# Optimization experiments

Measured on AMD Instinct MI355X. Metric: run time of the kernel, lower is better.

The kernel has to match this reference:

```python
import jax, jax.numpy as jnp
import numpy as np

NUM_HEADS = 4


def setup_inputs() -> dict:
    key = jax.random.key(0)
    ks = jax.random.split(key, 4)
    B, C, H, W = 8, 128, 128, 128
    x = jax.random.normal(ks[0], (B, C, H, W), dtype=jnp.float32)
    w_qkv = jax.random.normal(ks[1], (3 * C, C), dtype=jnp.float32) * 0.05
    w_proj = jax.random.normal(ks[2], (C, C), dtype=jnp.float32) * 0.05
    w_dw = jax.random.normal(ks[3], (C, 1, 3, 3), dtype=jnp.float32) * 0.1
    gamma = jnp.asarray(0.1, dtype=jnp.float32)
    return {"x": x, "w_qkv": w_qkv, "w_proj": w_proj, "w_dw": w_dw, "gamma": gamma}


def reference(x, w_qkv, w_proj, w_dw, gamma):
    B, C, H, W = x.shape
    h = NUM_HEADS
    d = C // h
    scale = d ** (-0.5)

    # 1x1 conv qkv: [B,3C,H,W]
    qkv = jnp.einsum('oc,bchw->bohw', w_qkv, x)
    # split and reshape to [B,h,H,W,d]; channel index = head*d + dim
    def to_heads(t):
        return t.reshape(B, h, d, H, W).transpose(0, 1, 3, 4, 2)
    q = to_heads(qkv[:, :C])
    k = to_heads(qkv[:, C:2 * C])
    v = to_heads(qkv[:, 2 * C:])

    # H-axis attention: attend along W within each row i
    attn_h = jnp.einsum('bhijd,bhizd->bhijz', q * scale, k)  # [B,h,H,W,W]
    idx_w = jnp.arange(W, dtype=jnp.float32)
    decay_w = jnp.exp(-gamma * jnp.abs(idx_w[:, None] - idx_w[None, :]))  # [W,W]
    attn_h = jax.nn.softmax(attn_h, axis=-1) * decay_w
    out_h = jnp.einsum('bhijz,bhizd->bhijd', attn_h, v)  # [B,h,H,W,d]

    # W-axis attention: attend along H within each column
    qw = q.transpose(0, 1, 3, 2, 4)  # [B,h,W,H,d]
    kw = k.transpose(0, 1, 3, 2, 4)
    vw = v.transpose(0, 1, 3, 2, 4)
    attn_w = jnp.einsum('bhwjd,bhwzd->bhwjz', qw * scale, kw)  # [B,h,W,H,H]
    idx_h = jnp.arange(H, dtype=jnp.float32)
    decay_h = jnp.exp(-gamma * jnp.abs(idx_h[:, None] - idx_h[None, :]))  # [H,H]
    attn_w = jax.nn.softmax(attn_w, axis=-1) * decay_h
    out_w = jnp.einsum('bhwjz,bhwzd->bhwjd', attn_w, vw).transpose(0, 1, 3, 2, 4)

    out = out_h + out_w  # [B,h,H,W,d]
    # back to [B,C,H,W], channel = head*d + dim
    out = out.transpose(0, 1, 4, 2, 3).reshape(B, C, H, W)

    # LePE: depthwise 3x3 conv (replaces out, matching original code)
    out = jax.lax.conv_general_dilated(
        out, w_dw, window_strides=(1, 1), padding='SAME',
        feature_group_count=C,
        dimension_numbers=('NCHW', 'OIHW', 'NCHW'))

    # 1x1 proj
    out = jnp.einsum('oc,bchw->bohw', w_proj, out)
    return out
```

## Files before the change

kernel.cpp:

```cpp
#include <hip/hip_runtime.h>

typedef unsigned short u16;
typedef unsigned int   u32;
typedef short bf16x8 __attribute__((ext_vector_type(8)));
typedef float f32x4  __attribute__((ext_vector_type(4)));
typedef float f32x2  __attribute__((ext_vector_type(2)));

#define B_   8
#define C_   128
#define H_   128
#define W_   128
#define NH   4
#define D_   32
#define HW_  16384
#define SCALE 0.17677669529663687f
#define SCL2E 0.2550437602866803f

__device__ __forceinline__ float bf2f_u(u16 u) { union { u32 i; float f; } x; x.i = ((u32)u) << 16; return x.f; }
__device__ __forceinline__ float bflo(u32 u)   { union { u32 i; float f; } x; x.i = u << 16; return x.f; }
__device__ __forceinline__ float bfhi(u32 u)   { union { u32 i; float f; } x; x.i = u & 0xffff0000u; return x.f; }
__device__ __forceinline__ u16   f2bf(float f) {
  union { float f; u32 i; } x; x.f = f;
  u32 i = x.i;
  return (u16)((i + 0x7fffu + ((i >> 16) & 1u)) >> 16);
}
__device__ __forceinline__ u32 pk2(float a, float b) {
  return (u32)f2bf(a) | ((u32)f2bf(b) << 16);
}
__device__ __forceinline__ u32 cvtpk(float a, float b) {
  u32 r;
  asm("v_cvt_pk_bf16_f32 %0, %1, %2" : "=v"(r) : "v"(a), "v"(b));
  return r;
}
__device__ __forceinline__ bf16x8 ld_frag_g(const u16* p) {
  union { uint4 u; bf16x8 f; } c; c.u = *(const uint4*)p; return c.f;
}

__global__ __launch_bounds__(256) void k_wcvt2(const float* __restrict__ wq,
                                               const float* __restrict__ wp,
                                               u16* __restrict__ dq,
                                               u16* __restrict__ dp) {
  int i = blockIdx.x * 256 + threadIdx.x;
  const float* src; u16* dst; int j;
  if (i < 12288) { src = wq; dst = dq; j = i; }
  else           { src = wp; dst = dp; j = i - 12288; }
  float4 v = ((const float4*)src)[j];
  uint2 st; st.x = pk2(v.x, v.y); st.y = pk2(v.z, v.w);
  *(uint2*)(dst + (size_t)j * 4) = st;
}

__global__ __launch_bounds__(256) void k_qkv(const float* __restrict__ x,
                                             const u16* __restrict__ wqb,
                                             u16* __restrict__ qkvb) {
  __shared__ u32 tile[8704];
  const int tid = threadIdx.x, w = tid >> 6, lane = tid & 63;
  const int c16 = lane & 15, rg = lane >> 4;
  const int b = blockIdx.z;
  const int P0 = blockIdx.x * 128;
  const float* sb = x + (size_t)b * C_ * HW_ + P0;

  #pragma unroll
  for (int ci = 0; ci < 4; ++ci) {
    int cp = 16 * w + 4 * ci + rg;
    #pragma unroll
    for (int ph = 0; ph < 2; ++ph) {
      int p = 4 * c16 + 64 * ph;
      const float* r0 = sb + (size_t)(2 * cp) * HW_ + p;
      float4 a  = *(const float4*)r0;
      float4 bb = *(const float4*)(r0 + HW_);
      tile[(p + 0) * 65 + cp] = pk2(a.x, bb.x);
      tile[(p + 1) * 65 + cp] = pk2(a.y, bb.y);
      tile[(p + 2) * 65 + cp] = pk2(a.z, bb.z);
      tile[(p + 3) * 65 + cp] = pk2(a.w, bb.w);
    }
  }
  __syncthreads();

  const int pw = w * 32;
  bf16x8 bfr[2][4];
  #pragma unroll
  for (int nt = 0; nt < 2; ++nt)
    #pragma unroll
    for (int kk = 0; kk < 4; ++kk) {
      int p = pw + nt * 16 + c16;
      int cp0 = kk * 16 + rg * 4;
      union { u32 d[4]; bf16x8 f; } u;
      u.d[0] = tile[p * 65 + cp0];
      u.d[1] = tile[p * 65 + cp0 + 1];
      u.d[2] = tile[p * 65 + cp0 + 2];
      u.d[3] = tile[p * 65 + cp0 + 3];
      bfr[nt][kk] = u.f;
    }
  __syncthreads();

  u32* eb = tile + w * 544;

  const int p0 = P0 + pw;
  const f32x4 zero = {0.f, 0.f, 0.f, 0.f};
  #pragma unroll 1
  for (int pass = 0; pass < 3; ++pass) {
    {
      const u16* wsrc = wqb + (size_t)pass * 16384;
      #pragma unroll
      for (int j = 0; j < 8; ++j) {
        int idx = tid + 256 * j;
        uint4 v = *(const uint4*)(wsrc + idx * 8);
        *(uint4*)(tile + (idx >> 4) * 68 + (idx & 15) * 4) = v;
      }
    }
    __syncthreads();

    f32x4 acc[8][2];
    #pragma unroll
    for (int mt = 0; mt < 8; ++mt) { acc[mt][0] = zero; acc[mt][1] = zero; }

    #pragma unroll
    for (int kk = 0; kk < 4; ++kk) {
      #pragma unroll
      for (int mt = 0; mt < 8; ++mt) {
        union { uint4 u; bf16x8 f; } afu;
        afu.u = *(const uint4*)(tile + (mt * 16 + c16) * 68 + kk * 16 + rg * 4);
        acc[mt][0] = __builtin_amdgcn_mfma_f32_16x16x32_bf16(afu.f, bfr[0][kk], acc[mt][0], 0, 0, 0);
        acc[mt][1] = __builtin_amdgcn_mfma_f32_16x16x32_bf16(afu.f, bfr[1][kk], acc[mt][1], 0, 0, 0);
      }
    }
    __syncthreads();

    u16* ob = qkvb + (size_t)pass * ((size_t)B_ * NH * HW_ * D_);
    #pragma unroll
    for (int h = 0; h < 4; ++h) {
      #pragma unroll
      for (int m2 = 0; m2 < 2; ++m2) {
        #pragma unroll
        for (int nt = 0; nt < 2; ++nt) {
          f32x4 oa = acc[2 * h + m2][nt];
          int pixl = nt * 16 + c16;
          int dp = m2 * 8 + rg * 2;
          eb[pixl * 17 + dp]     = cvtpk(oa[0], oa[1]);
          eb[pixl * 17 + dp + 1] = cvtpk(oa[2], oa[3]);
        }
      }
      #pragma unroll
      for (int s = 0; s < 2; ++s) {
        int pixl = s * 16 + (lane >> 2);
        const u32* src = eb + pixl * 17 + (lane & 3) * 4;
        uint4 v; v.x = src[0]; v.y = src[1]; v.z = src[2]; v.w = src[3];
        *(uint4*)(ob + ((size_t)(b * NH + h) * HW_ + p0 + pixl) * 32 + (lane & 3) * 8) = v;
      }
    }
    __syncthreads();
  }
}

__global__ __launch_bounds__(256) void k_proj(const u16* __restrict__ cv,
                                              const u16* __restrict__ wpb,
                                              float* __restrict__ out) {
  __shared__ u32 tile[8704];
  const int tid = threadIdx.x, w = tid >> 6, lane = tid & 63;
  const int c16 = lane & 15, rg = lane >> 4;
  const int b = blockIdx.z;
  const int P0 = blockIdx.x * 128;
  const u16* sb = cv + (size_t)b * C_ * HW_ + P0;

  #pragma unroll
  for (int ci = 0; ci < 4; ++ci) {
    int cp = 16 * w + 4 * ci + rg;
    #pragma unroll
    for (int ph = 0; ph < 2; ++ph) {
      int p = 4 * c16 + 64 * ph;
      const u16* r0 = sb + (size_t)(2 * cp) * HW_ + p;
      uint2 a  = *(const uint2*)r0;
      uint2 bb = *(const uint2*)(r0 + HW_);
      tile[(p + 0) * 65 + cp] = (a.x & 0xffffu) | (bb.x << 16);
      tile[(p + 1) * 65 + cp] = (a.x >> 16)     | (bb.x & 0xffff0000u);
      tile[(p + 2) * 65 + cp] = (a.y & 0xffffu) | (bb.y << 16);
      tile[(p + 3) * 65 + cp] = (a.y >> 16)     | (bb.y & 0xffff0000u);
    }
  }
  __syncthreads();

  const int pw = w * 32;
  bf16x8 bfr[2][4];
  #pragma unroll
  for (int nt = 0; nt < 2; ++nt)
    #pragma unroll
    for (int kk = 0; kk < 4; ++kk) {
      int p = pw + nt * 16 + c16;
      int cp0 = kk * 16 + rg * 4;
      union { u32 d[4]; bf16x8 f; } u;
      u.d[0] = tile[p * 65 + cp0];
      u.d[1] = tile[p * 65 + cp0 + 1];
      u.d[2] = tile[p * 65 + cp0 + 2];
      u.d[3] = tile[p * 65 + cp0 + 3];
      bfr[nt][kk] = u.f;
    }
  __syncthreads();

  u32* eb = tile + w * 544;

  #pragma unroll
  for (int j = 0; j < 8; ++j) {
    int idx = tid + 256 * j;
    uint4 v = *(const uint4*)(wpb + idx * 8);
    *(uint4*)(tile + (idx >> 4) * 68 + (idx & 15) * 4) = v;
  }
  __syncthreads();

  const int p0 = P0 + pw;
  const f32x4 zero = {0.f, 0.f, 0.f, 0.f};
  f32x4 acc[8][2];
  #pragma unroll
  for (int mt = 0; mt < 8; ++mt) { acc[mt][0] = zero; acc[mt][1] = zero; }

  #pragma unroll
  for (int kk = 0; kk < 4; ++kk) {
    #pragma unroll
    for (int mt = 0; mt < 8; ++mt) {
      union { uint4 u; bf16x8 f; } afu;
      afu.u = *(const uint4*)(tile + (mt * 16 + c16) * 68 + kk * 16 + rg * 4);
      acc[mt][0] = __builtin_amdgcn_mfma_f32_16x16x32_bf16(afu.f, bfr[0][kk], acc[mt][0], 0, 0, 0);
      acc[mt][1] = __builtin_amdgcn_mfma_f32_16x16x32_bf16(afu.f, bfr[1][kk], acc[mt][1], 0, 0, 0);
    }
  }
  __syncthreads();

  float* ob = out + (size_t)b * C_ * HW_;
  #pragma unroll
  for (int mt = 0; mt < 8; ++mt) {
    #pragma unroll
    for (int nt = 0; nt < 2; ++nt) {
      f32x4 oa = acc[mt][nt];
      int pixl = nt * 16 + c16;
      #pragma unroll
      for (int r = 0; r < 4; ++r) {
        union { float f; u32 u; } cu; cu.f = oa[r];
        eb[(rg * 4 + r) * 33 + pixl] = cu.u;
      }
    }
    #pragma unroll
    for (int s = 0; s < 2; ++s) {
      int ol = s * 8 + (lane >> 3);
      int px = (lane & 7) * 4;
      const u32* src = eb + ol * 33 + px;
      uint4 v; v.x = src[0]; v.y = src[1]; v.z = src[2]; v.w = src[3];
      *(uint4*)(ob + (size_t)(mt * 16 + ol) * HW_ + p0 + px) = v;
    }
  }
}

__global__ __launch_bounds__(256) void k_attn_mfma(const u16* __restrict__ qb,
                                                   const u16* __restrict__ kb,
                                                   const u16* __restrict__ vb,
                                                   const float* __restrict__ gp,
                                                   u16* __restrict__ houtb,
                                                   u16* __restrict__ woutb) {
  __shared__ u32 lds[4][16 * 68 + 32 * 18];
  const int tid  = threadIdx.x;
  const int w    = tid >> 6;
  const int lane = tid & 63;
  const int head = blockIdx.y & 3;
  const int axis = blockIdx.y >> 2;
  const int b    = blockIdx.z;
  const int line = blockIdx.x * 4 + w;
  u32* vt = &lds[w][0];
  u32* pt = &lds[w][0];
  u32* ot = &lds[w][16 * 68];
  const size_t base = (size_t)(b * NH + head) * HW_ * D_;
  const float g = gp[0];
  const int c16 = lane & 15, rg = lane >> 4;
  const size_t pstride = axis ? (size_t)128 * D_ : (size_t)D_;
  const size_t lbase   = base + (size_t)line * (axis ? D_ : 128 * D_);

  u32 v0r[16], v1r[16];
  {
    const u16* v0p = vb + lbase + (size_t)(2 * lane) * pstride;
    const u16* v1p = v0p + pstride;
    #pragma unroll
    for (int t = 0; t < 4; ++t) {
      *(uint4*)&v0r[4 * t] = *(const uint4*)(v0p + 8 * t);
      *(uint4*)&v1r[4 * t] = *(const uint4*)(v1p + 8 * t);
    }
  }

  bf16x8 kf[8];
  #pragma unroll
  for (int nt = 0; nt < 8; ++nt)
    kf[nt] = ld_frag_g(kb + lbase + (size_t)(nt * 16 + c16) * pstride + rg * 8);

  bf16x8 vf[2][4];
  #pragma unroll
  for (int ph = 0; ph < 2; ++ph) {
    #pragma unroll
    for (int dw = 0; dw < 8; ++dw) {
      u32 a = v0r[ph * 8 + dw], bq = v1r[ph * 8 + dw];
      u32 lo = (a & 0xffffu) | (bq << 16);
      u32 hi = (a >> 16) | (bq & 0xffff0000u);
      vt[(2 * dw) * 68 + lane]     = lo;
      vt[(2 * dw + 1) * 68 + lane] = hi;
    }
    #pragma unroll
    for (int t = 0; t < 4; ++t) {
      union { uint4 u; bf16x8 f; } c;
      c.u = *(const uint4*)(vt + c16 * 68 + t * 16 + rg * 4);
      vf[ph][t] = c.f;
    }
  }

  const float R1v  = __expf(-g),        Ri1v  = __expf(g);
  const float R12v = __expf(-12.f * g), Ri12v = __expf(12.f * g);
  const float R16v = __expf(-16.f * g), Ri16v = __expf(16.f * g);
  const f32x2 R1p   = {R1v,  Ri1v};
  const f32x2 R12p  = {R12v, Ri12v};
  const f32x2 R16ip = {Ri16v, R16v};
  float t0 = (float)(rg * 4 - c16);
  f32x2 F2 = {__expf(-g * t0), __expf(g * t0)};

  u16* ob = axis ? woutb : houtb;
  const f32x4 zero = {0.f, 0.f, 0.f, 0.f};

  bf16x8 qf = ld_frag_g(qb + lbase + (size_t)c16 * pstride + rg * 8);

  #pragma unroll 1
  for (int mt = 0; mt < 8; ++mt) {
    int mtn = mt < 7 ? mt + 1 : 7;
    bf16x8 qf_n = ld_frag_g(qb + lbase + (size_t)(mtn * 16 + c16) * pstride + rg * 8);

    f32x4 sa[8];
    __builtin_amdgcn_s_setprio(1);
    #pragma unroll
    for (int nt = 0; nt < 8; ++nt)
      sa[nt] = __builtin_amdgcn_mfma_f32_16x16x32_bf16(kf[nt], qf, zero, 0, 0, 0);
    __builtin_amdgcn_s_setprio(0);

    f32x2 l2 = {0.f, 0.f};
    #pragma unroll
    for (int nt = 0; nt < 8; ++nt) {
      f32x4 s4 = sa[nt] * SCL2E;
      float e0 = __builtin_amdgcn_exp2f(s4[0]);
      float e1 = __builtin_amdgcn_exp2f(s4[1]);
      float e2 = __builtin_amdgcn_exp2f(s4[2]);
      float e3 = __builtin_amdgcn_exp2f(s4[3]);
      sa[nt][0] = e0; sa[nt][1] = e1; sa[nt][2] = e2; sa[nt][3] = e3;
      l2 += (f32x2){e0, e1};
      l2 += (f32x2){e2, e3};
    }
    float l = l2[0] + l2[1];
    l += __shfl_xor(l, 16);
    l += __shfl_xor(l, 32);
    float linv = __builtin_amdgcn_rcpf(l);

    f32x2 ffi = F2 * linv;
    #pragma unroll
    for (int nt = 0; nt < 8; ++nt) {
      float d0 = fminf(ffi[0], ffi[1]); ffi *= R1p;
      float d1 = fminf(ffi[0], ffi[1]); ffi *= R1p;
      float d2 = fminf(ffi[0], ffi[1]); ffi *= R1p;
      float d3 = fminf(ffi[0], ffi[1]); ffi *= R1p;
      ffi *= R12p;
      f32x2 p01 = (f32x2){sa[nt][0], sa[nt][1]} * (f32x2){d0, d1};
      f32x2 p23 = (f32x2){sa[nt][2], sa[nt][3]} * (f32x2){d2, d3};
      uint2 st;
      st.x = cvtpk(p01[0], p01[1]);
      st.y = cvtpk(p23[0], p23[1]);
      *(uint2*)(pt + c16 * 68 + nt * 8 + rg * 2) = st;
    }
    F2 *= R16ip;

    f32x4 oa0 = zero, oa1 = zero;
    __builtin_amdgcn_s_setprio(1);
    #pragma unroll
    for (int t = 0; t < 4; ++t) {
      union { uint4 u; bf16x8 f; } af;
      af.u = *(const uint4*)(pt + c16 * 68 + t * 16 + rg * 4);
      oa0 = __builtin_amdgcn_mfma_f32_16x16x32_bf16(af.f, vf[0][t], oa0, 0, 0, 0);
      oa1 = __builtin_amdgcn_mfma_f32_16x16x32_bf16(af.f, vf[1][t], oa1, 0, 0, 0);
    }
    __builtin_amdgcn_s_setprio(0);

    {
      int mo = mt & 1;
      uint2 st0, st1;
      st0.x = cvtpk(oa0[0], oa0[1]); st0.y = cvtpk(oa0[2], oa0[3]);
      st1.x = cvtpk(oa1[0], oa1[1]); st1.y = cvtpk(oa1[2], oa1[3]);
      *(uint2*)(ot + c16 * 18 + mo * 8 + rg * 2)        = st0;
      *(uint2*)(ot + (16 + c16) * 18 + mo * 8 + rg * 2) = st1;
      if (mo) {
        int zb = (mt >> 1) * 32;
        int q = lane & 3;
        #pragma unroll
        for (int s = 0; s < 2; ++s) {
          int d = s * 16 + (lane >> 2);
          const u32* src = ot + d * 18 + q * 4;
          uint4 v; v.x = src[0]; v.y = src[1]; v.z = src[2]; v.w = src[3];
          *(uint4*)(ob + ((size_t)(b * C_ + head * D_ + d) * 128 + line) * 128 + zb + q * 8) = v;
        }
      }
    }
    qf = qf_n;
  }
}

__global__ __launch_bounds__(256) void k_conv(const u16* __restrict__ hb,
                                              const u16* __restrict__ wb,
                                              const float* __restrict__ wdw,
                                              u16* __restrict__ convo) {
  __shared__ u16 t[128 * 136];
  const int tid = threadIdx.x;
  const int c = blockIdx.x, b = blockIdx.y;
  const size_t pb = (size_t)(b * C_ + c) * HW_;

  for (int i = tid; i < 2048; i += 256) {
    int e = i * 8; int r = e >> 7, col = e & 127;
    *(uint4*)&t[r * 136 + col] = *(const uint4*)(hb + pb + e);
  }
  __syncthreads();

  {
    const int p = tid & 63;
    const int hc0 = (tid >> 6) * 32;
    u32* tw = (u32*)t;
    u32 w0[16], w1[16];
    const u16* r0 = wb + pb + (size_t)(2 * p) * 128 + hc0;
    const u16* r1 = r0 + 128;
    #pragma unroll
    for (int q = 0; q < 4; ++q) {
      *(uint4*)&w0[4 * q] = *(const uint4*)(r0 + 8 * q);
      *(uint4*)&w1[4 * q] = *(const uint4*)(r1 + 8 * q);
    }
    #pragma unroll
    for (int k = 0; k < 32; ++k) {
      u32 d = tw[(hc0 + k) * 68 + p];
      u32 wa = (k & 1) ? (w0[k >> 1] & 0xffff0000u) : (w0[k >> 1] << 16);
      u32 wc = (k & 1) ? (w1[k >> 1] & 0xffff0000u) : (w1[k >> 1] << 16);
      union { u32 u; float f; } fa, fc;
      fa.u = wa; fc.u = wc;
      f32x2 s = (f32x2){bflo(d) + fa.f, bfhi(d) + fc.f};
      tw[(hc0 + k) * 68 + p] = cvtpk(s[0], s[1]);
    }
  }
  __syncthreads();

  float k9[9];
  #pragma unroll
  for (int i = 0; i < 9; ++i) k9[i] = wdw[c * 9 + i];

  for (int px = tid; px < HW_; px += 256) {
    int r = px >> 7, col = px & 127;
    float a = 0.f;
    #pragma unroll
    for (int di = 0; di < 3; ++di) {
      int rr = r + di - 1;
      if (rr < 0 || rr > 127) continue;
      #pragma unroll
      for (int dj = 0; dj < 3; ++dj) {
        int cc2 = col + dj - 1;
        if (cc2 < 0 || cc2 > 127) continue;
        a += k9[di * 3 + dj] * bf2f_u(t[rr * 136 + cc2]);
      }
    }
    convo[pb + px] = f2bf(a);
  }
}

extern "C" void kernel_launch(void* const* d_in, const int* in_sizes, int n_in,
                              void* d_out, int out_size, void* d_ws, size_t ws_size,
                              hipStream_t stream) {
  const float* x     = (const float*)d_in[0];
  const float* wqkv  = (const float*)d_in[1];
  const float* wproj = (const float*)d_in[2];
  const float* wdw   = (const float*)d_in[3];
  const float* gamma = (const float*)d_in[4];
  float* out = (float*)d_out;
  char* ws = (char*)d_ws;

  u16* q   = (u16*)(ws);
  u16* k   = (u16*)(ws + 33554432ull);
  u16* v   = (u16*)(ws + 67108864ull);
  u16* hb  = (u16*)(ws + 100663296ull);
  u16* wb  = (u16*)(ws + 134217728ull);
  u16* cv  = (u16*)(ws + 167772160ull);
  u16* wqb = (u16*)(ws + 201326592ull);
  u16* wpb = (u16*)(ws + 201326592ull + 131072ull);

  k_wcvt2    <<<dim3(64),        256, 0, stream>>>(wqkv, wproj, wqb, wpb);
  k_qkv      <<<dim3(128, 1, 8), 256, 0, stream>>>(x, wqb, q);
  k_attn_mfma<<<dim3(32, 8, 8),  256, 0, stream>>>(q, k, v, gamma, hb, wb);
  k_conv     <<<dim3(128, 8),    256, 0, stream>>>(hb, wb, wdw, cv);
  k_proj     <<<dim3(128, 1, 8), 256, 0, stream>>>(cv, wpb, out);
}
```

Before: 263.3 us.

## Software-pipeline QK MFMA with PV stage and vectorize depthwise conv

The attention loop is software-pipelined: the next tile's QK^T MFMAs are issued alongside the current tile's PV MFMAs, the Q fragment is prefetched two tiles ahead, and the output store is deferred by one iteration with an epilogue for the last tile. This aims to overlap matrix-core work with the exp/softmax VALU work and hide store latency, at the cost of more live registers. The depthwise 3x3 conv now computes 8 contiguous outputs per thread using a 16-byte LDS load and packed 16-byte global stores, replacing per-pixel scalar loads and 2-byte stores.

After: 246.4 us. 6.4% less time.

```diff
diff --git a/kernel.cpp b/kernel.cpp
--- a/kernel.cpp
+++ b/kernel.cpp
@@ -319,19 +319,18 @@
   const f32x4 zero = {0.f, 0.f, 0.f, 0.f};
 
   bf16x8 qf = ld_frag_g(qb + lbase + (size_t)c16 * pstride + rg * 8);
+  f32x4 sa[8];
+  __builtin_amdgcn_s_setprio(1);
+  #pragma unroll
+  for (int nt = 0; nt < 8; ++nt)
+    sa[nt] = __builtin_amdgcn_mfma_f32_16x16x32_bf16(kf[nt], qf, zero, 0, 0, 0);
+  __builtin_amdgcn_s_setprio(0);
+  qf = ld_frag_g(qb + lbase + (size_t)(16 + c16) * pstride + rg * 8);
+
+  f32x4 oap0 = zero, oap1 = zero;
 
   #pragma unroll 1
   for (int mt = 0; mt < 8; ++mt) {
-    int mtn = mt < 7 ? mt + 1 : 7;
-    bf16x8 qf_n = ld_frag_g(qb + lbase + (size_t)(mtn * 16 + c16) * pstride + rg * 8);
-
-    f32x4 sa[8];
-    __builtin_amdgcn_s_setprio(1);
-    #pragma unroll
-    for (int nt = 0; nt < 8; ++nt)
-      sa[nt] = __builtin_amdgcn_mfma_f32_16x16x32_bf16(kf[nt], qf, zero, 0, 0, 0);
-    __builtin_amdgcn_s_setprio(0);
-
     f32x2 l2 = {0.f, 0.f};
     #pragma unroll
     for (int nt = 0; nt < 8; ++nt) {
@@ -366,8 +365,13 @@
     }
     F2 *= R16ip;
 
+    __builtin_amdgcn_s_setprio(1);
+    if (mt < 7) {
+      #pragma unroll
+      for (int nt = 0; nt < 8; ++nt)
+        sa[nt] = __builtin_amdgcn_mfma_f32_16x16x32_bf16(kf[nt], qf, zero, 0, 0, 0);
+    }
     f32x4 oa0 = zero, oa1 = zero;
-    __builtin_amdgcn_s_setprio(1);
     #pragma unroll
     for (int t = 0; t < 4; ++t) {
       union { uint4 u; bf16x8 f; } af;
@@ -376,16 +380,21 @@
       oa1 = __builtin_amdgcn_mfma_f32_16x16x32_bf16(af.f, vf[1][t], oa1, 0, 0, 0);
     }
     __builtin_amdgcn_s_setprio(0);
-
-    {
-      int mo = mt & 1;
+    if (mt < 7) {
+      int qi = mt + 2 > 7 ? 7 : mt + 2;
+      qf = ld_frag_g(qb + lbase + (size_t)(qi * 16 + c16) * pstride + rg * 8);
+    }
+
+    if (mt > 0) {
+      int pm = mt - 1;
+      int mo = pm & 1;
       uint2 st0, st1;
-      st0.x = cvtpk(oa0[0], oa0[1]); st0.y = cvtpk(oa0[2], oa0[3]);
-      st1.x = cvtpk(oa1[0], oa1[1]); st1.y = cvtpk(oa1[2], oa1[3]);
+      st0.x = cvtpk(oap0[0], oap0[1]); st0.y = cvtpk(oap0[2], oap0[3]);
+      st1.x = cvtpk(oap1[0], oap1[1]); st1.y = cvtpk(oap1[2], oap1[3]);
       *(uint2*)(ot + c16 * 18 + mo * 8 + rg * 2)        = st0;
       *(uint2*)(ot + (16 + c16) * 18 + mo * 8 + rg * 2) = st1;
       if (mo) {
-        int zb = (mt >> 1) * 32;
+        int zb = (pm >> 1) * 32;
         int q = lane & 3;
         #pragma unroll
         for (int s = 0; s < 2; ++s) {
@@ -396,7 +405,23 @@
         }
       }
     }
-    qf = qf_n;
+    oap0 = oa0; oap1 = oa1;
+  }
+
+  {
+    uint2 st0, st1;
+    st0.x = cvtpk(oap0[0], oap0[1]); st0.y = cvtpk(oap0[2], oap0[3]);
+    st1.x = cvtpk(oap1[0], oap1[1]); st1.y = cvtpk(oap1[2], oap1[3]);
+    *(uint2*)(ot + c16 * 18 + 8 + rg * 2)        = st0;
+    *(uint2*)(ot + (16 + c16) * 18 + 8 + rg * 2) = st1;
+    int q = lane & 3;
+    #pragma unroll
+    for (int s = 0; s < 2; ++s) {
+      int d = s * 16 + (lane >> 2);
+      const u32* src = ot + d * 18 + q * 4;
+      uint4 v; v.x = src[0]; v.y = src[1]; v.z = src[2]; v.w = src[3];
+      *(uint4*)(ob + ((size_t)(b * C_ + head * D_ + d) * 128 + line) * 128 + 96 + q * 8) = v;
+    }
   }
 }
 
@@ -444,21 +469,37 @@
   #pragma unroll
   for (int i = 0; i < 9; ++i) k9[i] = wdw[c * 9 + i];
 
-  for (int px = tid; px < HW_; px += 256) {
-    int r = px >> 7, col = px & 127;
-    float a = 0.f;
+  for (int ch = tid; ch < 2048; ch += 256) {
+    int r = ch >> 4;
+    int c0 = (ch & 15) << 3;
+    float a0 = 0.f, a1 = 0.f, a2 = 0.f, a3 = 0.f;
+    float a4 = 0.f, a5 = 0.f, a6 = 0.f, a7 = 0.f;
     #pragma unroll
     for (int di = 0; di < 3; ++di) {
       int rr = r + di - 1;
       if (rr < 0 || rr > 127) continue;
-      #pragma unroll
-      for (int dj = 0; dj < 3; ++dj) {
-        int cc2 = col + dj - 1;
-        if (cc2 < 0 || cc2 > 127) continue;
-        a += k9[di * 3 + dj] * bf2f_u(t[rr * 136 + cc2]);
-      }
-    }
-    convo[pb + px] = f2bf(a);
+      const u16* row = &t[rr * 136 + c0];
+      union { uint4 u; u16 h[8]; } m;
+      m.u = *(const uint4*)row;
+      float v0 = c0 ? bf2f_u(row[-1]) : 0.f;
+      float v1 = bf2f_u(m.h[0]), v2 = bf2f_u(m.h[1]), v3 = bf2f_u(m.h[2]);
+      float v4 = bf2f_u(m.h[3]), v5 = bf2f_u(m.h[4]), v6 = bf2f_u(m.h[5]);
+      float v7 = bf2f_u(m.h[6]), v8 = bf2f_u(m.h[7]);
+      float v9 = (c0 < 120) ? bf2f_u(row[8]) : 0.f;
+      float ka = k9[di * 3], kb2 = k9[di * 3 + 1], kc = k9[di * 3 + 2];
+      a0 += ka * v0 + kb2 * v1 + kc * v2;
+      a1 += ka * v1 + kb2 * v2 + kc * v3;
+      a2 += ka * v2 + kb2 * v3 + kc * v4;
+      a3 += ka * v3 + kb2 * v4 + kc * v5;
+      a4 += ka * v4 + kb2 * v5 + kc * v6;
+      a5 += ka * v5 + kb2 * v6 + kc * v7;
+      a6 += ka * v6 + kb2 * v7 + kc * v8;
+      a7 += ka * v7 + kb2 * v8 + kc * v9;
+    }
+    uint4 st;
+    st.x = cvtpk(a0, a1); st.y = cvtpk(a2, a3);
+    st.z = cvtpk(a4, a5); st.w = cvtpk(a6, a7);
+    *(uint4*)(convo + pb + r * 128 + c0) = st;
   }
 }
 
```
